# Optimization experiments

Measured on AMD Instinct MI355X. Metric: run time of the kernel, lower is better.

## Reference

```python
import jax, jax.numpy as jnp
import numpy as np

A_MIN = 0.001
EPS = 1e-08


def setup_inputs() -> dict:
    key = jax.random.key(0)
    k1, k2, k3, k4 = jax.random.split(key, 4)
    B, O, I = 512, 1024, 512
    x = jax.random.normal(k1, (B, I), dtype=jnp.float32)
    translation = jax.random.uniform(k2, (O, I), dtype=jnp.float32, minval=-1.0, maxval=1.0)
    scale_raw = jax.random.uniform(k3, (O, I), dtype=jnp.float32, minval=-2.0, maxval=0.0)
    weights = jax.random.normal(k4, (O, I), dtype=jnp.float32) * (1.0 / np.sqrt(I))
    return {"x": x, "translation": translation, "scale_raw": scale_raw, "weights": weights}


def reference(x, translation, scale_raw, weights):
    # x: (B, I); params: (O, I)
    scale = A_MIN + jax.nn.softplus(scale_raw)  # (O, I)
    # s: (B, O, I) broadcast intermediate
    s = (x[:, None, :] - translation[None, :, :]) / (scale[None, :, :] + EPS)
    s2 = s * s
    wavelet = (1.0 - s2) * jnp.exp(-0.5 * s2)  # mexican hat
    y = jnp.einsum('oi,boi->bo', weights, wavelet)  # reduce over in_features
    return y
```

## Files before the change

### kernel.cpp

```cpp
#include <hip/hip_runtime.h>


#define WL_A_MIN 0.001f
#define WL_EPS   1e-8f

constexpr int WL_B = 512;
constexpr int WL_O = 1024;
constexpr int WL_I = 512;

#define WL_SQK  0.84932180553704583800f
#define WL_IK   1.38629436111989061883f
#define WL_L2E  1.44269504088896340736f
#define WL_LN2  0.69314718055994530942f

typedef float v2f __attribute__((ext_vector_type(2)));

struct P3 { float nti, inv, w; };

__device__ __forceinline__ float fast_exp2(float a) {
#if __has_builtin(__builtin_amdgcn_exp2f)
    return __builtin_amdgcn_exp2f(a);
#else
    return exp2f(a);
#endif
}
__device__ __forceinline__ float fast_log2(float a) {
#if __has_builtin(__builtin_amdgcn_logf)
    return __builtin_amdgcn_logf(a);
#else
    return __log2f(a);
#endif
}
__device__ __forceinline__ float fast_rcp(float a) {
#if __has_builtin(__builtin_amdgcn_rcpf)
    return __builtin_amdgcn_rcpf(a);
#else
    return 1.0f / a;
#endif
}

__global__ __launch_bounds__(256) void wl_prep(
    const float* __restrict__ translation,
    const float* __restrict__ scale_raw,
    const float* __restrict__ weights,
    v2f* __restrict__ A2,
    float* __restrict__ W1)
{
    __shared__ P3 lds[16 * 64];
    const int t  = threadIdx.x;
    const int o0 = blockIdx.x * 64;
    const int i0 = blockIdx.y * 16;

    {
        const int o_l = t >> 2;
        const int iq  = t & 3;
        const size_t g = (size_t)(o0 + o_l) * WL_I + (i0 + iq * 4);
        const float4 tv = *reinterpret_cast<const float4*>(translation + g);
        const float4 sv = *reinterpret_cast<const float4*>(scale_raw   + g);
        const float4 wv = *reinterpret_cast<const float4*>(weights     + g);
        const float tt[4] = {tv.x, tv.y, tv.z, tv.w};
        const float ss[4] = {sv.x, sv.y, sv.z, sv.w};
        const float ww[4] = {wv.x, wv.y, wv.z, wv.w};
        #pragma unroll
        for (int j = 0; j < 4; ++j) {
            float ex  = fast_exp2(ss[j] * WL_L2E);
            float sp  = fast_log2(1.0f + ex) * WL_LN2;
            float inv = fast_rcp(WL_A_MIN + sp + WL_EPS) * WL_SQK;
            P3 pv; pv.nti = -tt[j] * inv; pv.inv = inv; pv.w = ww[j];
            lds[(iq * 4 + j) * 64 + o_l] = pv;
        }
    }
    __syncthreads();
    {
        const int o_l = t & 63;
        const int r   = t >> 6;
        const int o   = o0 + o_l;
        #pragma unroll
        for (int j = 0; j < 4; ++j) {
            const int i_l = r * 4 + j;
            P3 a = lds[i_l * 64 + o_l];
            A2[(size_t)(i0 + i_l) * WL_O + o] = (v2f){a.nti, a.inv};
            W1[(size_t)(i0 + i_l) * WL_O + o] = a.w;
        }
    }
}

__global__ __launch_bounds__(512, 8) void wl_main(
    const float* __restrict__ x,
    const v2f* __restrict__ A2,
    const float* __restrict__ W1,
    float* __restrict__ out)
{
    __shared__ float smem[8 * 513];

    const int tid  = threadIdx.x;
    const int lane = tid & 63;
    const int wid  = tid >> 6;
    const int o    = blockIdx.x * 64 + lane;
    const int b0   = blockIdx.y * 8;

    {
        const int b_l = tid & 7;
        const int seg = tid >> 3;
        const float* xg = &x[(size_t)(b0 + b_l) * WL_I + seg * 8];
        const float4 v0 = *reinterpret_cast<const float4*>(xg);
        const float4 v1 = *reinterpret_cast<const float4*>(xg + 4);
        const int base = seg * 64 + b_l;
        smem[base +  0] = v0.x;
        smem[base +  8] = v0.y;
        smem[base + 16] = v0.z;
        smem[base + 24] = v0.w;
        smem[base + 32] = v1.x;
        smem[base + 40] = v1.y;
        smem[base + 48] = v1.z;
        smem[base + 56] = v1.w;
    }
    __syncthreads();

    const v2f*   __restrict__ pA = A2 + (size_t)(wid * 64) * WL_O + o;
    const float* __restrict__ pW = W1 + (size_t)(wid * 64) * WL_O + o;
    const float* xr = &smem[wid * 64 * 8];

    float acc[8] = {0.f, 0.f, 0.f, 0.f, 0.f, 0.f, 0.f, 0.f};

    #pragma unroll 4
    for (int ii = 0; ii < 64; ++ii) {
        const v2f pa = *pA;  pA += WL_O;
        const float w = *pW;  pW += WL_O;
        const float mwk = w * (-WL_IK);
        const float nti = pa.x, inv = pa.y;
        const float4 xa = ((const float4*)xr)[0];
        const float4 xb = ((const float4*)xr)[1];
        xr += 8;
        const float xs[8] = {xa.x, xa.y, xa.z, xa.w, xb.x, xb.y, xb.z, xb.w};
        #pragma unroll
        for (int b = 0; b < 8; ++b) {
            float s_, u_, v_, e_;
            asm("v_fma_f32 %0, %1, %2, %3"
                : "=v"(s_) : "v"(xs[b]), "v"(inv), "v"(nti));
            asm("v_mul_f32 %0, %1, %1"
                : "=v"(u_) : "v"(s_));
            e_ = fast_exp2(-u_);
            asm("v_fma_f32 %0, %1, %2, %3"
                : "=v"(v_) : "v"(mwk), "v"(u_), "v"(w));
            asm("v_fma_f32 %0, %1, %2, %0"
                : "+v"(acc[b]) : "v"(v_), "v"(e_));
        }
    }

    __syncthreads();
    {
        const int c = wid * 64 + lane;
        #pragma unroll
        for (int k = 0; k < 8; ++k)
            smem[k * 513 + c] = acc[k];
    }
    __syncthreads();
    {
        float y = 0.f;
        #pragma unroll
        for (int sw = 0; sw < 8; ++sw)
            y += smem[wid * 513 + sw * 64 + lane];
        out[(size_t)(b0 + wid) * WL_O + o] = y;
    }
}

extern "C" void kernel_launch(void* const* d_in, const int* in_sizes, int n_in,
                              void* d_out, int out_size, void* d_ws, size_t ws_size,
                              hipStream_t stream) {
    const float* x           = (const float*)d_in[0];
    const float* translation = (const float*)d_in[1];
    const float* scale_raw   = (const float*)d_in[2];
    const float* weights     = (const float*)d_in[3];
    float*       out         = (float*)d_out;
    v2f*   A2 = (v2f*)d_ws;
    float* W1 = (float*)((char*)d_ws + (size_t)WL_I * WL_O * sizeof(v2f));

    wl_prep<<<dim3(WL_O / 64, WL_I / 16), dim3(256), 0, stream>>>(
        translation, scale_raw, weights, A2, W1);

    wl_main<<<dim3(WL_O / 64, WL_B / 8), dim3(512), 0, stream>>>(
        x, A2, W1, out);
}
```

Measured before the change: 111.0 us.

## Widen main kernel to 16 batch rows per block with 1024 threads

The main kernel now covers 16 batch rows per block with 16 waves, each wave reducing over 32 input features instead of 64. Each loaded parameter triple (nti, inv, w) is reused across twice as many batch rows, which halves the parameter traffic per output. The cross-wave reduction is reworked into two passes through shared memory so all 16 accumulators fit in the 8192-float buffer. In exchange there are more registers per thread and more barriers, and the larger blocks may lower occupancy. The kernel stays bound by transcendental math either way.

```diff
diff --git a/kernel.cpp b/kernel.cpp
--- a/kernel.cpp
+++ b/kernel.cpp
@@ -85,82 +85,90 @@
     }
 }
 
-__global__ __launch_bounds__(512, 8) void wl_main(
+__global__ __launch_bounds__(1024, 8) void wl_main(
     const float* __restrict__ x,
     const v2f* __restrict__ A2,
     const float* __restrict__ W1,
     float* __restrict__ out)
 {
-    __shared__ float smem[8 * 513];
+    __shared__ float smem[8192];
 
     const int tid  = threadIdx.x;
     const int lane = tid & 63;
     const int wid  = tid >> 6;
     const int o    = blockIdx.x * 64 + lane;
-    const int b0   = blockIdx.y * 8;
+    const int b0   = blockIdx.y * 16;
 
     {
-        const int b_l = tid & 7;
-        const int seg = tid >> 3;
+        const int b_l = tid & 15;
+        const int seg = tid >> 4;
         const float* xg = &x[(size_t)(b0 + b_l) * WL_I + seg * 8];
         const float4 v0 = *reinterpret_cast<const float4*>(xg);
         const float4 v1 = *reinterpret_cast<const float4*>(xg + 4);
-        const int base = seg * 64 + b_l;
-        smem[base +  0] = v0.x;
-        smem[base +  8] = v0.y;
-        smem[base + 16] = v0.z;
-        smem[base + 24] = v0.w;
-        smem[base + 32] = v1.x;
-        smem[base + 40] = v1.y;
-        smem[base + 48] = v1.z;
-        smem[base + 56] = v1.w;
+        const int base = seg * 8 * 16 + b_l;
+        smem[base + 0 * 16] = v0.x;
+        smem[base + 1 * 16] = v0.y;
+        smem[base + 2 * 16] = v0.z;
+        smem[base + 3 * 16] = v0.w;
+        smem[base + 4 * 16] = v1.x;
+        smem[base + 5 * 16] = v1.y;
+        smem[base + 6 * 16] = v1.z;
+        smem[base + 7 * 16] = v1.w;
     }
     __syncthreads();
 
-    const v2f*   __restrict__ pA = A2 + (size_t)(wid * 64) * WL_O + o;
-    const float* __restrict__ pW = W1 + (size_t)(wid * 64) * WL_O + o;
-    const float* xr = &smem[wid * 64 * 8];
+    const v2f*   __restrict__ pA = A2 + (size_t)(wid * 32) * WL_O + o;
+    const float* __restrict__ pW = W1 + (size_t)(wid * 32) * WL_O + o;
+    const float* xrow = &smem[wid * 32 * 16];
 
-    float acc[8] = {0.f, 0.f, 0.f, 0.f, 0.f, 0.f, 0.f, 0.f};
+    float acc[16] = {0.f,0.f,0.f,0.f, 0.f,0.f,0.f,0.f,
+                     0.f,0.f,0.f,0.f, 0.f,0.f,0.f,0.f};
 
     #pragma unroll 4
-    for (int ii = 0; ii < 64; ++ii) {
-        const v2f pa = *pA;  pA += WL_O;
-        const float w = *pW;  pW += WL_O;
+    for (int ii = 0; ii < 32; ++ii) {
+        const v2f   pa = pA[(size_t)ii * WL_O];
+        const float w  = pW[(size_t)ii * WL_O];
         const float mwk = w * (-WL_IK);
         const float nti = pa.x, inv = pa.y;
-        const float4 xa = ((const float4*)xr)[0];
-        const float4 xb = ((const float4*)xr)[1];
-        xr += 8;
-        const float xs[8] = {xa.x, xa.y, xa.z, xa.w, xb.x, xb.y, xb.z, xb.w};
+        const float4* xf = reinterpret_cast<const float4*>(xrow + ii * 16);
         #pragma unroll
-        for (int b = 0; b < 8; ++b) {
-            float s_, u_, v_, e_;
-            asm("v_fma_f32 %0, %1, %2, %3"
-                : "=v"(s_) : "v"(xs[b]), "v"(inv), "v"(nti));
-            asm("v_mul_f32 %0, %1, %1"
-                : "=v"(u_) : "v"(s_));
-            e_ = fast_exp2(-u_);
-            asm("v_fma_f32 %0, %1, %2, %3"
-                : "=v"(v_) : "v"(mwk), "v"(u_), "v"(w));
-            asm("v_fma_f32 %0, %1, %2, %0"
-                : "+v"(acc[b]) : "v"(v_), "v"(e_));
+        for (int q = 0; q < 4; ++q) {
+            const float4 xq = xf[q];
+            const float xs[4] = {xq.x, xq.y, xq.z, xq.w};
+            #pragma unroll
+            for (int j = 0; j < 4; ++j) {
+                const int b = q * 4 + j;
+                const float s = fmaf(xs[j], inv, nti);
+                const float u = s * s;
+                const float e = fast_exp2(-u);
+                const float v = fmaf(mwk, u, w);
+                acc[b] = fmaf(v, e, acc[b]);
+            }
         }
     }
 
     __syncthreads();
-    {
-        const int c = wid * 64 + lane;
+    #pragma unroll
+    for (int k = 0; k < 8; ++k)
+        smem[(wid * 8 + k) * 64 + lane] = acc[k];
+    __syncthreads();
+    if (wid < 8) {
+        float y = 0.f;
         #pragma unroll
-        for (int k = 0; k < 8; ++k)
-            smem[k * 513 + c] = acc[k];
+        for (int src = 0; src < 16; ++src)
+            y += smem[(src * 8 + wid) * 64 + lane];
+        out[(size_t)(b0 + wid) * WL_O + o] = y;
     }
     __syncthreads();
-    {
+    #pragma unroll
+    for (int k = 0; k < 8; ++k)
+        smem[(wid * 8 + k) * 64 + lane] = acc[8 + k];
+    __syncthreads();
+    if (wid >= 8) {
         float y = 0.f;
         #pragma unroll
-        for (int sw = 0; sw < 8; ++sw)
-            y += smem[wid * 513 + sw * 64 + lane];
+        for (int src = 0; src < 16; ++src)
+            y += smem[(src * 8 + (wid - 8)) * 64 + lane];
         out[(size_t)(b0 + wid) * WL_O + o] = y;
     }
 }
@@ -179,6 +187,6 @@
     wl_prep<<<dim3(WL_O / 64, WL_I / 16), dim3(256), 0, stream>>>(
         translation, scale_raw, weights, A2, W1);
 
-    wl_main<<<dim3(WL_O / 64, WL_B / 8), dim3(512), 0, stream>>>(
+    wl_main<<<dim3(WL_O / 64, WL_B / 16), dim3(1024), 0, stream>>>(
         x, A2, W1, out);
 }
```

Result: faster. 104.6 us (-5.8%).

## Retile main kernel: lanes over batch, params broadcast from LDS in interleaved tiles

Applied to the files above, without the earlier changes.

Reorganizes the main kernel so each lane owns a batch row and each wave handles two output features. Per-(o,i) parameters are packed by the prep kernel into interleaved (nti, inv, w) chunks and staged through LDS, where all lanes read them as broadcasts, while x is staged transposed per 32-wide input chunk. This removes the cross-wave shared-memory reduction and the per-element strided global parameter loads, at the cost of 16 loop iterations that each need two block barriers. Occupancy is lowered to 4 waves per SIMD, and the prep kernel now writes an uncoalesced stride-3 layout.

```diff
diff --git a/kernel.cpp b/kernel.cpp
--- a/kernel.cpp
+++ b/kernel.cpp
@@ -12,10 +12,6 @@
 #define WL_IK   1.38629436111989061883f
 #define WL_L2E  1.44269504088896340736f
 #define WL_LN2  0.69314718055994530942f
-
-typedef float v2f __attribute__((ext_vector_type(2)));
-
-struct P3 { float nti, inv, w; };
 
 __device__ __forceinline__ float fast_exp2(float a) {
 #if __has_builtin(__builtin_amdgcn_exp2f)
@@ -39,130 +35,107 @@
 #endif
 }
 
+__device__ __forceinline__ void wl_elem(float nti, float inv, float w,
+                                        float xv, float& acc) {
+    const float s = fmaf(xv, inv, nti);
+    const float u = s * s;
+    const float e = fast_exp2(-u);
+    const float h = fmaf(-WL_IK, u, 1.0f);
+    acc = fmaf(w * h, e, acc);
+}
+
+#define WL_Q(ACC, OSEL, Q)                                                    \
+  {                                                                           \
+    const float4* P4_ = reinterpret_cast<const float4*>(Pl);                  \
+    const int bse_ = (wid * 2 + (OSEL)) * 24 + (Q) * 6;                       \
+    const float4 a0 = P4_[bse_ + 0], a1 = P4_[bse_ + 1], a2 = P4_[bse_ + 2];  \
+    const float4 a3 = P4_[bse_ + 3], a4 = P4_[bse_ + 4], a5 = P4_[bse_ + 5];  \
+    wl_elem(a0.x, a0.y, a0.z, xr[(Q) * 8 + 0], ACC);                          \
+    wl_elem(a0.w, a1.x, a1.y, xr[(Q) * 8 + 1], ACC);                          \
+    wl_elem(a1.z, a1.w, a2.x, xr[(Q) * 8 + 2], ACC);                          \
+    wl_elem(a2.y, a2.z, a2.w, xr[(Q) * 8 + 3], ACC);                          \
+    wl_elem(a3.x, a3.y, a3.z, xr[(Q) * 8 + 4], ACC);                          \
+    wl_elem(a3.w, a4.x, a4.y, xr[(Q) * 8 + 5], ACC);                          \
+    wl_elem(a4.z, a4.w, a5.x, xr[(Q) * 8 + 6], ACC);                          \
+    wl_elem(a5.y, a5.z, a5.w, xr[(Q) * 8 + 7], ACC);                          \
+  }
+
 __global__ __launch_bounds__(256) void wl_prep(
     const float* __restrict__ translation,
     const float* __restrict__ scale_raw,
     const float* __restrict__ weights,
-    v2f* __restrict__ A2,
-    float* __restrict__ W1)
+    float* __restrict__ P)
 {
-    __shared__ P3 lds[16 * 64];
-    const int t  = threadIdx.x;
-    const int o0 = blockIdx.x * 64;
-    const int i0 = blockIdx.y * 16;
-
-    {
-        const int o_l = t >> 2;
-        const int iq  = t & 3;
-        const size_t g = (size_t)(o0 + o_l) * WL_I + (i0 + iq * 4);
-        const float4 tv = *reinterpret_cast<const float4*>(translation + g);
-        const float4 sv = *reinterpret_cast<const float4*>(scale_raw   + g);
-        const float4 wv = *reinterpret_cast<const float4*>(weights     + g);
-        const float tt[4] = {tv.x, tv.y, tv.z, tv.w};
-        const float ss[4] = {sv.x, sv.y, sv.z, sv.w};
-        const float ww[4] = {wv.x, wv.y, wv.z, wv.w};
-        #pragma unroll
-        for (int j = 0; j < 4; ++j) {
-            float ex  = fast_exp2(ss[j] * WL_L2E);
-            float sp  = fast_log2(1.0f + ex) * WL_LN2;
-            float inv = fast_rcp(WL_A_MIN + sp + WL_EPS) * WL_SQK;
-            P3 pv; pv.nti = -tt[j] * inv; pv.inv = inv; pv.w = ww[j];
-            lds[(iq * 4 + j) * 64 + o_l] = pv;
-        }
-    }
-    __syncthreads();
-    {
-        const int o_l = t & 63;
-        const int r   = t >> 6;
-        const int o   = o0 + o_l;
-        #pragma unroll
-        for (int j = 0; j < 4; ++j) {
-            const int i_l = r * 4 + j;
-            P3 a = lds[i_l * 64 + o_l];
-            A2[(size_t)(i0 + i_l) * WL_O + o] = (v2f){a.nti, a.inv};
-            W1[(size_t)(i0 + i_l) * WL_O + o] = a.w;
-        }
+    const int t   = threadIdx.x;
+    const int o   = blockIdx.x * 64 + (t >> 2);
+    const int i0  = blockIdx.y * 16 + (t & 3) * 4;
+    const size_t g = (size_t)o * WL_I + i0;
+    const float4 tv = *reinterpret_cast<const float4*>(translation + g);
+    const float4 sv = *reinterpret_cast<const float4*>(scale_raw   + g);
+    const float4 wv = *reinterpret_cast<const float4*>(weights     + g);
+    const float tt[4] = {tv.x, tv.y, tv.z, tv.w};
+    const float ss[4] = {sv.x, sv.y, sv.z, sv.w};
+    const float ww[4] = {wv.x, wv.y, wv.z, wv.w};
+    const int gx = o >> 4, o_l = o & 15;
+    #pragma unroll
+    for (int j = 0; j < 4; ++j) {
+        const int i  = i0 + j;
+        const int c  = i >> 5, i_l = i & 31;
+        const float ex  = fast_exp2(ss[j] * WL_L2E);
+        const float sp  = fast_log2(1.0f + ex) * WL_LN2;
+        const float inv = fast_rcp(WL_A_MIN + sp + WL_EPS) * WL_SQK;
+        const size_t off = ((((size_t)gx * 16 + c) * 16 + o_l) * 32 + i_l) * 3;
+        P[off + 0] = -tt[j] * inv;
+        P[off + 1] = inv;
+        P[off + 2] = ww[j];
     }
 }
 
-__global__ __launch_bounds__(512, 8) void wl_main(
+__global__ __launch_bounds__(512, 4) void wl_main(
     const float* __restrict__ x,
-    const v2f* __restrict__ A2,
-    const float* __restrict__ W1,
+    const float* __restrict__ P,
     float* __restrict__ out)
 {
-    __shared__ float smem[8 * 513];
+    __shared__ float xT[32 * 64];
+    __shared__ float Pl[16 * 32 * 3];
 
     const int tid  = threadIdx.x;
     const int lane = tid & 63;
     const int wid  = tid >> 6;
-    const int o    = blockIdx.x * 64 + lane;
-    const int b0   = blockIdx.y * 8;
+    const int gx   = blockIdx.x;
+    const int gy   = blockIdx.y;
+    const float* __restrict__ Pg = P + (size_t)gx * (16 * 512 * 3);
 
-    {
-        const int b_l = tid & 7;
-        const int seg = tid >> 3;
-        const float* xg = &x[(size_t)(b0 + b_l) * WL_I + seg * 8];
-        const float4 v0 = *reinterpret_cast<const float4*>(xg);
-        const float4 v1 = *reinterpret_cast<const float4*>(xg + 4);
-        const int base = seg * 64 + b_l;
-        smem[base +  0] = v0.x;
-        smem[base +  8] = v0.y;
-        smem[base + 16] = v0.z;
-        smem[base + 24] = v0.w;
-        smem[base + 32] = v1.x;
-        smem[base + 40] = v1.y;
-        smem[base + 48] = v1.z;
-        smem[base + 56] = v1.w;
-    }
-    __syncthreads();
+    float acc0 = 0.f, acc1 = 0.f;
+    float xr[32];
 
-    const v2f*   __restrict__ pA = A2 + (size_t)(wid * 64) * WL_O + o;
-    const float* __restrict__ pW = W1 + (size_t)(wid * 64) * WL_O + o;
-    const float* xr = &smem[wid * 64 * 8];
-
-    float acc[8] = {0.f, 0.f, 0.f, 0.f, 0.f, 0.f, 0.f, 0.f};
-
-    #pragma unroll 4
-    for (int ii = 0; ii < 64; ++ii) {
-        const v2f pa = *pA;  pA += WL_O;
-        const float w = *pW;  pW += WL_O;
-        const float mwk = w * (-WL_IK);
-        const float nti = pa.x, inv = pa.y;
-        const float4 xa = ((const float4*)xr)[0];
-        const float4 xb = ((const float4*)xr)[1];
-        xr += 8;
-        const float xs[8] = {xa.x, xa.y, xa.z, xa.w, xb.x, xb.y, xb.z, xb.w};
+    for (int c = 0; c < 16; ++c) {
+        __syncthreads();
+        if (tid < 384) {
+            reinterpret_cast<float4*>(Pl)[tid] =
+                reinterpret_cast<const float4*>(Pg + (size_t)c * 1536)[tid];
+        }
+        {
+            const int ig = tid >> 6;
+            const float4 v = *reinterpret_cast<const float4*>(
+                x + (size_t)(gy * 64 + lane) * WL_I + c * 32 + ig * 4);
+            xT[(ig * 4 + 0) * 64 + lane] = v.x;
+            xT[(ig * 4 + 1) * 64 + lane] = v.y;
+            xT[(ig * 4 + 2) * 64 + lane] = v.z;
+            xT[(ig * 4 + 3) * 64 + lane] = v.w;
+        }
+        __syncthreads();
         #pragma unroll
-        for (int b = 0; b < 8; ++b) {
-            float s_, u_, v_, e_;
-            asm("v_fma_f32 %0, %1, %2, %3"
-                : "=v"(s_) : "v"(xs[b]), "v"(inv), "v"(nti));
-            asm("v_mul_f32 %0, %1, %1"
-                : "=v"(u_) : "v"(s_));
-            e_ = fast_exp2(-u_);
-            asm("v_fma_f32 %0, %1, %2, %3"
-                : "=v"(v_) : "v"(mwk), "v"(u_), "v"(w));
-            asm("v_fma_f32 %0, %1, %2, %0"
-                : "+v"(acc[b]) : "v"(v_), "v"(e_));
-        }
+        for (int k = 0; k < 32; ++k)
+            xr[k] = xT[k * 64 + lane];
+        WL_Q(acc0, 0, 0) WL_Q(acc0, 0, 1) WL_Q(acc0, 0, 2) WL_Q(acc0, 0, 3)
+        WL_Q(acc1, 1, 0) WL_Q(acc1, 1, 1) WL_Q(acc1, 1, 2) WL_Q(acc1, 1, 3)
     }
 
-    __syncthreads();
-    {
-        const int c = wid * 64 + lane;
-        #pragma unroll
-        for (int k = 0; k < 8; ++k)
-            smem[k * 513 + c] = acc[k];
-    }
-    __syncthreads();
-    {
-        float y = 0.f;
-        #pragma unroll
-        for (int sw = 0; sw < 8; ++sw)
-            y += smem[wid * 513 + sw * 64 + lane];
-        out[(size_t)(b0 + wid) * WL_O + o] = y;
-    }
+    const int b = gy * 64 + lane;
+    const int o = gx * 16 + wid * 2;
+    out[(size_t)b * WL_O + o]     = acc0;
+    out[(size_t)b * WL_O + o + 1] = acc1;
 }
 
 extern "C" void kernel_launch(void* const* d_in, const int* in_sizes, int n_in,
@@ -173,12 +146,11 @@
     const float* scale_raw   = (const float*)d_in[2];
     const float* weights     = (const float*)d_in[3];
     float*       out         = (float*)d_out;
-    v2f*   A2 = (v2f*)d_ws;
-    float* W1 = (float*)((char*)d_ws + (size_t)WL_I * WL_O * sizeof(v2f));
+    float*       P           = (float*)d_ws;
 
     wl_prep<<<dim3(WL_O / 64, WL_I / 16), dim3(256), 0, stream>>>(
-        translation, scale_raw, weights, A2, W1);
+        translation, scale_raw, weights, P);
 
-    wl_main<<<dim3(WL_O / 64, WL_B / 8), dim3(512), 0, stream>>>(
-        x, A2, W1, out);
+    wl_main<<<dim3(WL_O / 16, WL_B / 64), dim3(512), 0, stream>>>(
+        x, P, out);
 }
```

Result: slower. 139.7 us (+25.8%).
